# Optimization experiments

Hardware: AMD Instinct MI355X
Metric: run time of the kernel (lower is better)

Reference implementation:

```python
import jax, jax.numpy as jnp
import numpy as np

N_PER = 20000   # nodes per node-type
NDIM = 3        # number of node types / feature lists
N = N_PER * NDIM
H = 256         # n_hidden
R = 5           # e_type (num relations)
C = 16          # n_class
E = 600000      # num edges
L = 2           # n_layers
LEA = 0.3       # LeakyReLU slope


def setup_inputs() -> dict:
    key = jax.random.key(0)
    ks = iter(jax.random.split(key, 64))
    def w(shape, s=0.05):
        return jax.random.normal(next(ks), shape, jnp.float32) * s
    inp = {}
    inp['feat0'] = jax.random.normal(next(ks), (N_PER, 100), jnp.float32)
    inp['feat1'] = jax.random.normal(next(ks), (N_PER, 300), jnp.float32)
    inp['feat2'] = jax.random.normal(next(ks), (N_PER, 768), jnp.float32)
    inp['src'] = jax.random.randint(next(ks), (E,), 0, N, jnp.int32)
    inp['dst'] = jax.random.randint(next(ks), (E,), 0, N, jnp.int32)
    inp['etypes'] = jax.random.randint(next(ks), (E,), 0, R, jnp.int32)
    # encoder 0: in_feat=100 <= 128 -> Linear(100,H), LReLU, Linear(H,H)
    inp['e0w1'] = w((100, H)); inp['e0b1'] = w((H,))
    inp['e0w2'] = w((H, H));   inp['e0b2'] = w((H,))
    # encoder 1: in_feat=300 <= 512 -> Linear(300,256), LReLU, Linear(256,H)
    inp['e1w1'] = w((300, 256)); inp['e1b1'] = w((256,))
    inp['e1w2'] = w((256, H));   inp['e1b2'] = w((H,))
    # encoder 2: in_feat=768 <= 1024 -> Linear(768,512), LReLU, Linear(512,256), LReLU, Linear(256,H)
    inp['e2w1'] = w((768, 512)); inp['e2b1'] = w((512,))
    inp['e2w2'] = w((512, 256)); inp['e2b2'] = w((256,))
    inp['e2w3'] = w((256, H));   inp['e2b3'] = w((H,))
    # RelGraphConv layers: per-relation weight, self-loop weight, bias
    inp['gW'] = w((L, R, H, H)); inp['gL'] = w((L, H, H)); inp['gB'] = w((L, H))
    # decoder: Linear(H,256), LReLU, Linear(256,C)
    inp['dw1'] = w((H, 256)); inp['db1'] = w((256,))
    inp['dw2'] = w((256, C)); inp['db2'] = w((C,))
    # constr_encoder: Linear(C,1024), LReLU, Linear(1024,H)
    inp['cew1'] = w((C, 1024)); inp['ceb1'] = w((1024,))
    inp['cew2'] = w((1024, H)); inp['ceb2'] = w((H,))
    # constr_decoder: Linear(H,256), LReLU, Linear(256,C)
    inp['cdw1'] = w((H, 256)); inp['cdb1'] = w((256,))
    inp['cdw2'] = w((256, C)); inp['cdb2'] = w((C,))
    return inp


def _lrelu(x):
    return jnp.where(x > 0, x, LEA * x)


def reference(feat0, feat1, feat2, e0w1, e0b1, e0w2, e0b2, e1w1, e1b1, e1w2, e1b2,
              e2w1, e2b1, e2w2, e2b2, e2w3, e2b3, gW, gL, gB,
              dw1, db1, dw2, db2, cew1, ceb1, cew2, ceb2, cdw1, cdb1, cdw2, cdb2,
              src, dst, etypes):
    # per-type encoders (dropout = identity at inference)
    h0 = _lrelu(feat0 @ e0w1 + e0b1) @ e0w2 + e0b2
    h1 = _lrelu(feat1 @ e1w1 + e1b1) @ e1w2 + e1b2
    h2 = _lrelu(_lrelu(feat2 @ e2w1 + e2b1) @ e2w2 + e2b2) @ e2w3 + e2b3
    h = jnp.concatenate([h0, h1, h2], axis=0)  # [N, H]
    n_nodes = h.shape[0]
    src64 = src.astype(jnp.int32)
    # RelGraphConv layers: m_e = W_{r(e)} h_src; h' = sum_in(m) + h @ W_loop + b
    for l in range(L):
        proj = jnp.einsum('nh,rhg->rng', h, gW[l])        # [R, N, H]
        msgs = proj[etypes, src64]                         # [E, H] relation-indexed gather
        agg = jax.ops.segment_sum(msgs, dst, num_segments=n_nodes)
        h = agg + h @ gL[l] + gB[l]
    feat = _lrelu(h @ dw1 + db1) @ dw2 + db2               # [N, C] decoder
    cf = _lrelu(feat @ cew1 + ceb1) @ cew2 + ceb2          # constr_encoder
    cf = _lrelu(cf @ cdw1 + cdb1) @ cdw2 + cdb2            # constr_decoder -> [N, C]
    con_loss = jnp.mean((cf - feat) ** 2)                  # reconstruction constraint loss
    # triple-nested loop == segment mean over the NDIM node-type blocks
    res = cf.reshape(NDIM, n_nodes // NDIM, C).mean(axis=0)  # [N/NDIM, C]
    return res, con_loss
```

## Files before the change

### kernel.cpp

```cpp
#include <hip/hip_runtime.h>
#include <stdint.h>

#define E_NUM 600000
#define N_NODES 60000
#define NPER 20000
#define NKEY 300000
#define MROW 60032
#define HPAD 60160
#define MP20 20096
#define KA 1536

typedef __attribute__((ext_vector_type(8))) short frag8;
typedef __attribute__((ext_vector_type(4))) float facc4;

__device__ __forceinline__ float bf2f(uint16_t u) {
  union { uint32_t i; float f; } v; v.i = ((uint32_t)u) << 16; return v.f;
}
__device__ __forceinline__ uint16_t f2bf(float f) {
  union { float f; uint32_t i; } v; v.f = f;
  uint32_t r = v.i + 0x7FFFu + ((v.i >> 16) & 1u);
  return (uint16_t)(r >> 16);
}
__device__ __forceinline__ uint16_t in2bf(const void* p, size_t i, int mode) {
  return mode ? f2bf(((const float*)p)[i]) : ((const uint16_t*)p)[i];
}

template<int ACT>
__global__ __launch_bounds__(256)
void gemm_bt(const uint16_t* __restrict__ A, int lda,
             const uint16_t* __restrict__ Bt, int ldb,
             const uint16_t* __restrict__ bias, uint16_t* __restrict__ C,
             int N, int K)
{
  __shared__ __align__(16) uint16_t sA[128 * 32];
  __shared__ __align__(16) uint16_t sB[128 * 32];
  const int tid = threadIdx.x;
  const int lane = tid & 63;
  const size_t mbase = (size_t)blockIdx.x * 128;
  const size_t nbase = (size_t)blockIdx.y * 128;
  const int wave = tid >> 6;
  const int wm = (wave >> 1) * 64;
  const int wn = (wave & 1) * 64;

  const uint16_t* Ab = A + mbase * lda;
  const uint16_t* Bb = Bt + nbase * ldb;

  facc4 acc[4][4] = {};

  const int nk = K >> 5;
  for (int kt = 0; kt < nk; ++kt) {
    const int kb = kt << 5;
#pragma unroll
    for (int it = 0; it < 2; ++it) {
      const int c = it * 256 + tid;
      const int r = c >> 2;
      const int kc = (c & 3) * 8;
      uint4 va = *(const uint4*)(Ab + (size_t)r * lda + kb + kc);
      uint4 vb = *(const uint4*)(Bb + (size_t)r * ldb + kb + kc);
      *(uint4*)(sA + (size_t)c * 8) = va;
      *(uint4*)(sB + (size_t)c * 8) = vb;
    }
    __syncthreads();
    {
      const int m15 = lane & 15, q8 = (lane >> 4) * 8;
      frag8 af[4], bfr[4];
#pragma unroll
      for (int i = 0; i < 4; ++i)
        af[i] = *(const frag8*)(sA + (size_t)(wm + i * 16 + m15) * 32 + q8);
#pragma unroll
      for (int j = 0; j < 4; ++j)
        bfr[j] = *(const frag8*)(sB + (size_t)(wn + j * 16 + m15) * 32 + q8);
#pragma unroll
      for (int i = 0; i < 4; ++i)
#pragma unroll
        for (int j = 0; j < 4; ++j)
          acc[i][j] = __builtin_amdgcn_mfma_f32_16x16x32_bf16(af[i], bfr[j], acc[i][j], 0, 0, 0);
    }
    __syncthreads();
  }

  const int m15 = lane & 15;
  const int r4 = (lane >> 4) * 4;
#pragma unroll
  for (int j = 0; j < 4; ++j) {
    const size_t col = nbase + wn + j * 16 + m15;
    const float bv = bias ? bf2f(bias[col]) : 0.f;
#pragma unroll
    for (int i = 0; i < 4; ++i) {
      const size_t row0 = mbase + wm + i * 16 + r4;
#pragma unroll
      for (int r = 0; r < 4; ++r) {
        float v = acc[i][j][r] + bv;
        if (ACT) v = v > 0.f ? v : 0.3f * v;
        C[(row0 + r) * (size_t)N + col] = f2bf(v);
      }
    }
  }
}

template<int MODE>
__global__ __launch_bounds__(256)
void gemv16_k(const uint16_t* __restrict__ A, const uint16_t* __restrict__ W,
              const uint16_t* __restrict__ bias, float* __restrict__ outf,
              uint16_t* __restrict__ padout)
{
  __shared__ float sW[256 * 16];
  for (int i = threadIdx.x; i < 4096; i += 256) sW[i] = bf2f(W[i]);
  __syncthreads();
  const int row = blockIdx.x * 16 + (threadIdx.x >> 4);
  const int col = threadIdx.x & 15;
  const uint16_t* ar = A + (size_t)row * 256;
  float acc = 0.f;
#pragma unroll
  for (int k = 0; k < 256; k += 8) {
    uint4 w4 = *(const uint4*)(ar + k);
    const uint16_t* pw = (const uint16_t*)&w4;
#pragma unroll
    for (int j = 0; j < 8; ++j) acc += bf2f(pw[j]) * sW[(k + j) * 16 + col];
  }
  acc += bf2f(bias[col]);
  outf[(size_t)row * 16 + col] = acc;
  if (MODE == 0) {
    padout[(size_t)row * 32 + col] = f2bf(acc);
    padout[(size_t)row * 32 + 16 + col] = 0;
  }
}

__global__ void probe_k(const uint16_t* __restrict__ f0, int* __restrict__ mode) {
  long i = (long)blockIdx.x * 256 + threadIdx.x;
  int bad = 0;
  for (; i < 2000000; i += (long)gridDim.x * 256)
    bad |= (((f0[i] >> 7) & 0xFFu) == 0xFFu);
  if (bad) atomicOr(mode, 1);
}

struct TDesc { const void* src; uint16_t* dst; long soff; int K, N, Kp, dstLd, dstOff; };
struct TPack { TDesc d[23]; int n; };

__global__ void transpose_k(TPack p, const int* __restrict__ modep) {
  const TDesc t = p.d[blockIdx.y];
  const int mode = *modep;
  const int total = t.N * t.Kp;
  for (int i = blockIdx.x * 256 + threadIdx.x; i < total; i += gridDim.x * 256) {
    const int n = i / t.Kp, k = i - n * t.Kp;
    t.dst[(size_t)n * t.dstLd + t.dstOff + k] =
        (k < t.K) ? in2bf(t.src, (size_t)(t.soff + (long)k * t.N + n), mode)
                  : (uint16_t)0;
  }
}

struct BDesc { const void* src; int n; int dstoff; };
struct BPack { BDesc d[16]; int n; };

__global__ void biasconv_k(BPack p, uint16_t* __restrict__ arena,
                           const int* __restrict__ modep) {
  const BDesc b = p.d[blockIdx.y];
  const int mode = *modep;
  for (int i = blockIdx.x * 256 + threadIdx.x; i < b.n; i += gridDim.x * 256)
    arena[b.dstoff + i] = in2bf(b.src, i, mode);
}

__global__ void repack_k(const void* __restrict__ in, uint16_t* __restrict__ out,
                         int row0, int Mvalid, int Kin, int Kpad, int rowsOut,
                         const int* __restrict__ modep)
{
  const int mode = *modep;
  const int total = rowsOut * Kpad;
  for (int i = blockIdx.x * 256 + threadIdx.x; i < total; i += gridDim.x * 256) {
    const int m = i / Kpad, k = i - m * Kpad;
    const int sm = row0 + m;
    out[i] = (sm < Mvalid && k < Kin) ? in2bf(in, (size_t)sm * Kin + k, mode)
                                      : (uint16_t)0;
  }
}

__global__ void zfill_k(uint16_t* p, int n) {
  int i = blockIdx.x * 256 + threadIdx.x;
  if (i < n) p[i] = 0;
}

__global__ void init_k(int* deg5, int* mode, float* lossAcc) {
  int i = blockIdx.x * 256 + threadIdx.x;
  if (i < NKEY) deg5[i] = 0;
  if (i == NKEY) { *mode = 0; *lossAcc = 0.f; }
}

__global__ void hist5_k(const int* __restrict__ dst, const int* __restrict__ ety,
                        int* __restrict__ deg5) {
  int e = blockIdx.x * 256 + threadIdx.x;
  if (e < E_NUM) atomicAdd(&deg5[dst[e] * 5 + ety[e]], 1);
}

__global__ __launch_bounds__(1024) void scan1_k(const int* __restrict__ deg,
                                                int* __restrict__ offs, int* __restrict__ bsum) {
  __shared__ int s[1024];
  const int i = blockIdx.x * 1024 + threadIdx.x;
  int v = (i < NKEY) ? deg[i] : 0;
  s[threadIdx.x] = v; __syncthreads();
  for (int d = 1; d < 1024; d <<= 1) {
    int x = (threadIdx.x >= d) ? s[threadIdx.x - d] : 0;
    __syncthreads();
    s[threadIdx.x] += x; __syncthreads();
  }
  if (i < NKEY) offs[i + 1] = s[threadIdx.x];
  if (threadIdx.x == 1023) bsum[blockIdx.x] = s[1023];
}

__global__ void scan2_k(int* bsum) {
  if (threadIdx.x == 0 && blockIdx.x == 0) {
    int run = 0;
    for (int b = 0; b < 293; ++b) { int t = bsum[b]; bsum[b] = run; run += t; }
  }
}

__global__ __launch_bounds__(1024) void scan3_k(const int* __restrict__ deg,
                                                int* __restrict__ offs, int* __restrict__ cursor,
                                                const int* __restrict__ bsum) {
  const int i = blockIdx.x * 1024 + threadIdx.x;
  if (i >= NKEY) return;
  const int t = offs[i + 1] + bsum[blockIdx.x];
  offs[i + 1] = t;
  cursor[i] = t - deg[i];
  if (i == 0) offs[0] = 0;
}

__global__ void scatter5_k(const int* __restrict__ src, const int* __restrict__ dst,
                           const int* __restrict__ ety, int* __restrict__ cursor,
                           int* __restrict__ payload) {
  int e = blockIdx.x * 256 + threadIdx.x;
  if (e >= E_NUM) return;
  int key = dst[e] * 5 + ety[e];
  int pos = atomicAdd(&cursor[key], 1);
  payload[pos] = src[e];
}

__global__ __launch_bounds__(256)
void gather_all_k(const uint16_t* __restrict__ h, const int* __restrict__ offs5,
                  const int* __restrict__ payload, uint16_t* __restrict__ Abuf)
{
  const int node = blockIdx.x * 4 + (threadIdx.x >> 6);
  const int lane = threadIdx.x & 63;
  uint16_t* arow = Abuf + (size_t)node * KA + lane * 4;
  if (node >= N_NODES) {
#pragma unroll
    for (int b = 0; b < 6; ++b) *(uint64_t*)(arow + b * 256) = 0;
    return;
  }
  *(uint64_t*)arow = *(const uint64_t*)(h + (size_t)node * 256 + lane * 4);
  const int base = node * 5;
#pragma unroll
  for (int r = 0; r < 5; ++r) {
    const int o0 = offs5[base + r], o1 = offs5[base + r + 1];
    float a0 = 0.f, a1 = 0.f, a2 = 0.f, a3 = 0.f;
    for (int e = o0; e < o1; ++e) {
      const int s = payload[e];
      uint64_t w = *(const uint64_t*)(h + (size_t)s * 256 + lane * 4);
      a0 += bf2f((uint16_t)w);         a1 += bf2f((uint16_t)(w >> 16));
      a2 += bf2f((uint16_t)(w >> 32)); a3 += bf2f((uint16_t)(w >> 48));
    }
    uint64_t o = (uint64_t)f2bf(a0) | ((uint64_t)f2bf(a1) << 16)
               | ((uint64_t)f2bf(a2) << 32) | ((uint64_t)f2bf(a3) << 48);
    *(uint64_t*)(arow + (1 + r) * 256) = o;
  }
}

__global__ void sentinel_k(uint16_t* out, float code) {
  int i = blockIdx.x * 256 + threadIdx.x;
  if (i > 320000) return;
  out[i] = (i == 0) ? f2bf(code) : (uint16_t)0;
}

__global__ __launch_bounds__(256) void loss_k(const float* __restrict__ cf,
                                              const float* __restrict__ feat,
                                              float* __restrict__ acc) {
  __shared__ float s[256];
  float p = 0.f;
  for (int i = blockIdx.x * 256 + threadIdx.x; i < N_NODES * 16; i += gridDim.x * 256) {
    float d = cf[i] - feat[i];
    p += d * d;
  }
  s[threadIdx.x] = p; __syncthreads();
  for (int d = 128; d > 0; d >>= 1) {
    if (threadIdx.x < d) s[threadIdx.x] += s[threadIdx.x + d];
    __syncthreads();
  }
  if (threadIdx.x == 0) atomicAdd(acc, s[0]);
}

__global__ void final_k(const float* __restrict__ cf, const float* __restrict__ lossAcc,
                        const int* __restrict__ modep, void* __restrict__ outv)
{
  int i = blockIdx.x * 256 + threadIdx.x;
  if (i > 320000) return;
  float v = (i == 320000) ? *lossAcc * (1.f / 960000.f)
                          : (cf[i] + cf[i + 320000] + cf[i + 640000]) * (1.f / 3.f);
  if (*modep) ((float*)outv)[i] = v;
  else ((uint16_t*)outv)[i] = f2bf(v);
}

extern "C" void kernel_launch(void* const* d_in, const int* in_sizes, int n_in,
                              void* d_out, int out_size, void* d_ws, size_t ws_size,
                              hipStream_t stream)
{
  (void)in_sizes; (void)n_in; (void)out_size;
  const void* feat0 = d_in[0];
  const void* feat1 = d_in[1];
  const void* feat2 = d_in[2];
  const int* srcI = (const int*)d_in[3];
  const int* dstI = (const int*)d_in[4];
  const int* etyI = (const int*)d_in[5];
  const void *e0w1 = d_in[6],  *e0b1 = d_in[7],  *e0w2 = d_in[8],  *e0b2 = d_in[9];
  const void *e1w1 = d_in[10], *e1b1 = d_in[11], *e1w2 = d_in[12], *e1b2 = d_in[13];
  const void *e2w1 = d_in[14], *e2b1 = d_in[15], *e2w2 = d_in[16], *e2b2 = d_in[17];
  const void *e2w3 = d_in[18], *e2b3 = d_in[19];
  const void *gW = d_in[20], *gL = d_in[21], *gB = d_in[22];
  const void *dw1 = d_in[23], *db1 = d_in[24], *dw2 = d_in[25], *db2 = d_in[26];
  const void *cew1 = d_in[27], *ceb1 = d_in[28], *cew2 = d_in[29], *ceb2 = d_in[30];
  const void *cdw1 = d_in[31], *cdb1 = d_in[32], *cdw2 = d_in[33], *cdb2 = d_in[34];

  uint8_t* base = (uint8_t*)d_ws;
  size_t off = 0;
  auto alloc = [&](size_t bytes) -> void* {
    void* p = base + off;
    off += (bytes + 255) & ~(size_t)255;
    return p;
  };
  int* modep    = (int*)alloc(4);
  int* bsum     = (int*)alloc(512 * 4);
  float* lossAcc = (float*)alloc(4);
  int* deg5    = (int*)alloc((size_t)NKEY * 4);
  int* offs5   = (int*)alloc((size_t)(NKEY + 33) * 4);
  int* cursor5 = (int*)alloc((size_t)NKEY * 4);
  int* payload = (int*)alloc((size_t)E_NUM * 4);
  auto wal = [&](size_t elems) { return (uint16_t*)alloc(elems * 2); };
  uint16_t* arena = wal(12576);
  uint16_t* e0w1t = wal(256 * 128);
  uint16_t* e0w2t = wal(256 * 256);
  uint16_t* e1w1t = wal(256 * 320);
  uint16_t* e1w2t = wal(256 * 256);
  uint16_t* e2w1t = wal(512 * 768);
  uint16_t* e2w2t = wal(256 * 512);
  uint16_t* e2w3t = wal(256 * 256);
  uint16_t* dw1t  = wal(256 * 256);
  uint16_t* cew1t = wal(1024 * 32);
  uint16_t* cew2t = wal(256 * 1024);
  uint16_t* cdw1t = wal(256 * 256);
  uint16_t* wall0 = wal(256 * KA);
  uint16_t* wall1 = wal(256 * KA);
  uint16_t* h1 = wal((size_t)HPAD * 256);
  uint16_t* h2 = wal((size_t)HPAD * 256);
  uint16_t* Abuf = wal((size_t)HPAD * KA);

  if (off > ws_size) {
    float wsmb = (float)(ws_size >> 20);
    if (wsmb > 512.f) wsmb = 512.f;
    sentinel_k<<<dim3(1251), 256, 0, stream>>>((uint16_t*)d_out, 10000.f + 16.f * wsmb);
    return;
  }

  enum { oE0B1 = 0, oE0B2 = 256, oE1B1 = 512, oE1B2 = 768, oE2B1 = 1024,
         oE2B2 = 1536, oE2B3 = 1792, oGB = 2048, oDB1 = 2560, oDB2 = 2816,
         oCEB1 = 2832, oCEB2 = 3856, oCDB1 = 4112, oCDB2 = 4368,
         oDW2 = 4384, oCDW2 = 8480 };

  uint16_t* f0p   = Abuf;
  uint16_t* eTmp0 = Abuf + 2572288;
  uint16_t* f1p   = Abuf;
  uint16_t* eTmp1 = Abuf + 6430720;
  uint16_t* f2p   = Abuf;
  uint16_t* tEnc  = Abuf + 15433728;
  uint16_t* eEnc  = Abuf + 25722880;
  uint16_t* Hc      = Abuf;
  uint16_t* featpad = Abuf + 61472768;
  float*    featf   = (float*)(Abuf + 63393792);
  float*    cff     = (float*)(Abuf + 67233792);

  init_k<<<dim3(1173), 256, 0, stream>>>(deg5, modep, lossAcc);
  probe_k<<<dim3(512), 256, 0, stream>>>((const uint16_t*)feat0, modep);
  hist5_k<<<dim3(2344), 256, 0, stream>>>(dstI, etyI, deg5);
  scan1_k<<<dim3(293), 1024, 0, stream>>>(deg5, offs5, bsum);
  scan2_k<<<dim3(1), 64, 0, stream>>>(bsum);
  scan3_k<<<dim3(293), 1024, 0, stream>>>(deg5, offs5, cursor5, bsum);
  scatter5_k<<<dim3(2344), 256, 0, stream>>>(srcI, dstI, etyI, cursor5, payload);

  BPack bp; int nb = 0;
  auto addB = [&](const void* s, int n, int dstoff) {
    bp.d[nb].src = s; bp.d[nb].n = n; bp.d[nb].dstoff = dstoff; ++nb;
  };
  addB(e0b1, 256, oE0B1); addB(e0b2, 256, oE0B2);
  addB(e1b1, 256, oE1B1); addB(e1b2, 256, oE1B2);
  addB(e2b1, 512, oE2B1); addB(e2b2, 256, oE2B2); addB(e2b3, 256, oE2B3);
  addB(gB, 512, oGB);
  addB(db1, 256, oDB1); addB(db2, 16, oDB2);
  addB(ceb1, 1024, oCEB1); addB(ceb2, 256, oCEB2);
  addB(cdb1, 256, oCDB1); addB(cdb2, 16, oCDB2);
  addB(dw2, 4096, oDW2); addB(cdw2, 4096, oCDW2);
  bp.n = nb;
  biasconv_k<<<dim3(16, nb), 256, 0, stream>>>(bp, arena, modep);

  TPack tp; int nd = 0;
  auto addT = [&](const void* s, long soff, uint16_t* d, int K, int N, int Kp,
                  int dstLd, int dstOff) {
    tp.d[nd].src = s; tp.d[nd].soff = soff; tp.d[nd].dst = d;
    tp.d[nd].K = K; tp.d[nd].N = N; tp.d[nd].Kp = Kp;
    tp.d[nd].dstLd = dstLd; tp.d[nd].dstOff = dstOff; ++nd;
  };
  addT(e0w1, 0, e0w1t, 100, 256, 128, 128, 0);
  addT(e0w2, 0, e0w2t, 256, 256, 256, 256, 0);
  addT(e1w1, 0, e1w1t, 300, 256, 320, 320, 0);
  addT(e1w2, 0, e1w2t, 256, 256, 256, 256, 0);
  addT(e2w1, 0, e2w1t, 768, 512, 768, 768, 0);
  addT(e2w2, 0, e2w2t, 512, 256, 512, 512, 0);
  addT(e2w3, 0, e2w3t, 256, 256, 256, 256, 0);
  addT(dw1,  0, dw1t,  256, 256, 256, 256, 0);
  addT(cew1, 0, cew1t, 16, 1024, 32, 32, 0);
  addT(cew2, 0, cew2t, 1024, 256, 1024, 1024, 0);
  addT(cdw1, 0, cdw1t, 256, 256, 256, 256, 0);
  uint16_t* walls[2] = { wall0, wall1 };
  for (int l = 0; l < 2; ++l) {
    addT(gL, (long)l * 65536, walls[l], 256, 256, 256, KA, 0);
    for (int r = 0; r < 5; ++r)
      addT(gW, (long)(l * 5 + r) * 65536, walls[l], 256, 256, 256, KA, 256 + r * 256);
  }
  tp.n = nd;
  transpose_k<<<dim3(48, nd), 256, 0, stream>>>(tp, modep);

  repack_k<<<dim3(2048), 256, 0, stream>>>(feat0, f0p, 0, NPER, 100, 128, MP20, modep);
  gemm_bt<1><<<dim3(157, 2), 256, 0, stream>>>(f0p, 128, e0w1t, 128, arena + oE0B1, eTmp0, 256, 128);
  gemm_bt<0><<<dim3(157, 2), 256, 0, stream>>>(eTmp0, 256, e0w2t, 256, arena + oE0B2, h1, 256, 256);
  repack_k<<<dim3(2048), 256, 0, stream>>>(feat1, f1p, 0, NPER, 300, 320, MP20, modep);
  gemm_bt<1><<<dim3(157, 2), 256, 0, stream>>>(f1p, 320, e1w1t, 320, arena + oE1B1, eTmp1, 256, 320);
  gemm_bt<0><<<dim3(157, 2), 256, 0, stream>>>(eTmp1, 256, e1w2t, 256, arena + oE1B2, h1 + (size_t)NPER * 256, 256, 256);
  repack_k<<<dim3(4096), 256, 0, stream>>>(feat2, f2p, 0, NPER, 768, 768, MP20, modep);
  gemm_bt<1><<<dim3(157, 4), 256, 0, stream>>>(f2p, 768, e2w1t, 768, arena + oE2B1, tEnc, 512, 768);
  gemm_bt<1><<<dim3(157, 2), 256, 0, stream>>>(tEnc, 512, e2w2t, 512, arena + oE2B2, eEnc, 256, 512);
  gemm_bt<0><<<dim3(157, 2), 256, 0, stream>>>(eEnc, 256, e2w3t, 256, arena + oE2B3,
                                               h1 + (size_t)2 * NPER * 256, 256, 256);

  uint16_t* hbuf[2] = { h1, h2 };
  for (int l = 0; l < 2; ++l) {
    uint16_t* hin  = hbuf[l & 1];
    uint16_t* hout = hbuf[(l + 1) & 1];
    gather_all_k<<<dim3(15040), 256, 0, stream>>>(hin, offs5, payload, Abuf);
    gemm_bt<0><<<dim3(469, 2), 256, 0, stream>>>(Abuf, KA, walls[l], KA,
                                                 arena + oGB + l * 256, hout, 256, KA);
  }

  gemm_bt<1><<<dim3(469, 2), 256, 0, stream>>>(h1, 256, dw1t, 256, arena + oDB1, h2, 256, 256);
  gemv16_k<0><<<dim3(3750), 256, 0, stream>>>(h2, arena + oDW2, arena + oDB2, featf, featpad);
  zfill_k<<<dim3(4), 256, 0, stream>>>(featpad + (size_t)N_NODES * 32, 32 * 32);

  gemm_bt<1><<<dim3(469, 8), 256, 0, stream>>>(featpad, 32, cew1t, 32, arena + oCEB1, Hc, 1024, 32);
  gemm_bt<0><<<dim3(469, 2), 256, 0, stream>>>(Hc, 1024, cew2t, 1024, arena + oCEB2, h1, 256, 1024);

  gemm_bt<1><<<dim3(469, 2), 256, 0, stream>>>(h1, 256, cdw1t, 256, arena + oCDB1, h2, 256, 256);
  gemv16_k<1><<<dim3(3750), 256, 0, stream>>>(h2, arena + oCDW2, arena + oCDB2, cff, nullptr);

  loss_k<<<dim3(512), 256, 0, stream>>>(cff, featf, lossAcc);
  final_k<<<dim3(1251), 256, 0, stream>>>(cff, lossAcc, modep, d_out);
}
```

Baseline: 1.052 ms.

## Use direct global-to-LDS loads in GEMM and split gather per relation

The GEMM tile loads now use the global_load_lds builtin, so data goes straight into shared memory instead of passing through registers. The gather kernel now gives one wave to each (node, relation) key rather than one wave per node looping over all five relations. That exposes more parallelism and balances the irregular edge loops better. The trade-off is six times as many waves, each doing less work, and a direct-LDS layout that depends on wave-contiguous addressing matching the earlier manual store layout.

```diff
diff --git a/kernel.cpp b/kernel.cpp
--- a/kernel.cpp
+++ b/kernel.cpp
@@ -23,6 +23,12 @@
 }
 __device__ __forceinline__ uint16_t in2bf(const void* p, size_t i, int mode) {
   return mode ? f2bf(((const float*)p)[i]) : ((const uint16_t*)p)[i];
+}
+
+typedef __attribute__((address_space(3))) uint32_t lds_u32;
+typedef const __attribute__((address_space(1))) uint32_t glb_u32;
+__device__ __forceinline__ void gl_lds16(const uint16_t* g, uint16_t* l) {
+  __builtin_amdgcn_global_load_lds((glb_u32*)g, (lds_u32*)l, 16, 0, 0);
 }
 
 template<int ACT>
@@ -55,10 +61,8 @@
       const int c = it * 256 + tid;
       const int r = c >> 2;
       const int kc = (c & 3) * 8;
-      uint4 va = *(const uint4*)(Ab + (size_t)r * lda + kb + kc);
-      uint4 vb = *(const uint4*)(Bb + (size_t)r * ldb + kb + kc);
-      *(uint4*)(sA + (size_t)c * 8) = va;
-      *(uint4*)(sB + (size_t)c * 8) = vb;
+      gl_lds16(Ab + (size_t)r * lda + kb + kc, sA + (size_t)(it * 256 + wave * 64) * 8);
+      gl_lds16(Bb + (size_t)r * ldb + kb + kc, sB + (size_t)(it * 256 + wave * 64) * 8);
     }
     __syncthreads();
     {
@@ -238,29 +242,31 @@
 void gather_all_k(const uint16_t* __restrict__ h, const int* __restrict__ offs5,
                   const int* __restrict__ payload, uint16_t* __restrict__ Abuf)
 {
-  const int node = blockIdx.x * 4 + (threadIdx.x >> 6);
+  const int w = blockIdx.x * 4 + (threadIdx.x >> 6);
   const int lane = threadIdx.x & 63;
-  uint16_t* arow = Abuf + (size_t)node * KA + lane * 4;
-  if (node >= N_NODES) {
-#pragma unroll
-    for (int b = 0; b < 6; ++b) *(uint64_t*)(arow + b * 256) = 0;
-    return;
-  }
-  *(uint64_t*)arow = *(const uint64_t*)(h + (size_t)node * 256 + lane * 4);
-  const int base = node * 5;
-#pragma unroll
-  for (int r = 0; r < 5; ++r) {
-    const int o0 = offs5[base + r], o1 = offs5[base + r + 1];
+  if (w < NKEY) {
+    const int node = w / 5, rel = w - node * 5;
+    const int o0 = offs5[w], o1 = offs5[w + 1];
     float a0 = 0.f, a1 = 0.f, a2 = 0.f, a3 = 0.f;
     for (int e = o0; e < o1; ++e) {
       const int s = payload[e];
-      uint64_t w = *(const uint64_t*)(h + (size_t)s * 256 + lane * 4);
-      a0 += bf2f((uint16_t)w);         a1 += bf2f((uint16_t)(w >> 16));
-      a2 += bf2f((uint16_t)(w >> 32)); a3 += bf2f((uint16_t)(w >> 48));
+      uint64_t v = *(const uint64_t*)(h + (size_t)s * 256 + lane * 4);
+      a0 += bf2f((uint16_t)v);         a1 += bf2f((uint16_t)(v >> 16));
+      a2 += bf2f((uint16_t)(v >> 32)); a3 += bf2f((uint16_t)(v >> 48));
     }
     uint64_t o = (uint64_t)f2bf(a0) | ((uint64_t)f2bf(a1) << 16)
                | ((uint64_t)f2bf(a2) << 32) | ((uint64_t)f2bf(a3) << 48);
-    *(uint64_t*)(arow + (1 + r) * 256) = o;
+    *(uint64_t*)(Abuf + (size_t)node * KA + (size_t)(1 + rel) * 256 + lane * 4) = o;
+  } else {
+    const int row = w - NKEY;
+    if (row >= HPAD) return;
+    uint16_t* arow = Abuf + (size_t)row * KA + lane * 4;
+    if (row < N_NODES) {
+      *(uint64_t*)arow = *(const uint64_t*)(h + (size_t)row * 256 + lane * 4);
+    } else {
+#pragma unroll
+      for (int b = 0; b < 6; ++b) *(uint64_t*)(arow + b * 256) = 0;
+    }
   }
 }
 
@@ -441,7 +447,7 @@
   for (int l = 0; l < 2; ++l) {
     uint16_t* hin  = hbuf[l & 1];
     uint16_t* hout = hbuf[(l + 1) & 1];
-    gather_all_k<<<dim3(15040), 256, 0, stream>>>(hin, offs5, payload, Abuf);
+    gather_all_k<<<dim3(90040), 256, 0, stream>>>(hin, offs5, payload, Abuf);
     gemm_bt<0><<<dim3(469, 2), 256, 0, stream>>>(Abuf, KA, walls[l], KA,
                                                  arena + oGB + l * 256, hout, 256, KA);
   }
```

After: 1.077 ms. +2.3%, slower.
